# Performance work log

Measured on AMD Instinct MI355X. Metric: run time of the kernel, lower is better.

The kernel has to match this reference:

```python
import jax, jax.numpy as jnp
import numpy as np

N_HEAD, D_MODEL, D_K, D_V, MAX_NEIGHBOR = 8, 512, 64, 64, 5
BS, SEQ = 2, 1024


def setup_inputs() -> dict:
    key = jax.random.key(0)
    ks = jax.random.split(key, 12)
    inp = {
        'q': jax.random.normal(ks[0], (BS, SEQ, D_MODEL), jnp.float32),
        'k': jax.random.normal(ks[1], (BS, SEQ, D_MODEL), jnp.float32),
        'v': jax.random.normal(ks[2], (BS, SEQ, D_MODEL), jnp.float32),
        'mask': jnp.ones((BS, SEQ, SEQ), jnp.int32),
        'dist': jax.random.randint(ks[3], (BS, SEQ, SEQ), 0, 10, jnp.int32),
        # weights stored as (in, out) so y = x @ W
        'w_qs': jax.random.normal(ks[4], (D_MODEL, N_HEAD * D_K), jnp.float32) * 0.02,
        'w_ks': jax.random.normal(ks[5], (D_MODEL, N_HEAD * D_K), jnp.float32) * 0.02,
        'w_vs': jax.random.normal(ks[6], (D_MODEL, N_HEAD * D_V), jnp.float32) * 0.02,
        'w_fc': jax.random.normal(ks[7], (N_HEAD * D_V, D_MODEL), jnp.float32) * 0.02,
        'ln_gamma': jnp.ones((D_MODEL,), jnp.float32),
        'ln_beta': jnp.zeros((D_MODEL,), jnp.float32),
        'base_rpr': jax.random.normal(ks[8], (MAX_NEIGHBOR + 1, D_K), jnp.float32) * 0.02,
    }
    return inp


def reference(q, k, v, mask, dist, w_qs, w_ks, w_vs, w_fc, ln_gamma, ln_beta, base_rpr):
    bs, sq, dm = q.shape
    temp = jnp.asarray(D_K, q.dtype) ** 0.5
    residual = q
    # layer norm on q only (as in original)
    mu = jnp.mean(q, axis=-1, keepdims=True)
    var = jnp.var(q, axis=-1, keepdims=True)
    qn = (q - mu) / jnp.sqrt(var + 1e-6) * ln_gamma + ln_beta
    # projections -> [bs, heads, seq, d]
    qh = (qn @ w_qs).reshape(bs, sq, N_HEAD, D_K).transpose(0, 2, 1, 3)
    kh = (k @ w_ks).reshape(bs, sq, N_HEAD, D_K).transpose(0, 2, 1, 3)
    vh = (v @ w_vs).reshape(bs, sq, N_HEAD, D_V).transpose(0, 2, 1, 3)
    qs = qh / temp
    # standard QK^T scores
    attn1 = jnp.einsum('bhid,bhjd->bhij', qs, kh)
    # relative-position scores: instead of materializing rpr[b,i,j,d],
    # contract q with the small base table then gather by clipped distance.
    dc = jnp.minimum(dist, MAX_NEIGHBOR)  # dist>max_neighbor -> max_neighbor
    qb = jnp.einsum('bhid,md->bhim', qs, base_rpr)  # [bs,h,seq,M+1]
    idx = jnp.broadcast_to(dc[:, None, :, :], (bs, N_HEAD, sq, sq))
    attn2 = jnp.take_along_axis(qb, idx, axis=-1)  # [bs,h,seq,seq]
    attn = attn1 + attn2
    attn = jnp.where(mask[:, None, :, :] == 0, jnp.asarray(-1e9, attn.dtype), attn)
    attn = jax.nn.softmax(attn, axis=-1)  # dropout disabled (eval)
    out = jnp.einsum('bhij,bhjd->bhid', attn, vh)
    out = out.transpose(0, 2, 1, 3).reshape(bs, sq, N_HEAD * D_V)
    out = out @ w_fc + residual
    return out, attn
```

## Files before the change

### kernel.cpp

```cpp
#include <hip/hip_runtime.h>
#include <math.h>

#define SEQ 1024
#define DM 512

typedef __attribute__((ext_vector_type(8))) short bf16x8;
typedef __attribute__((ext_vector_type(4))) short bf16x4;
typedef __attribute__((ext_vector_type(4))) float f32x4;
typedef __attribute__((ext_vector_type(4))) int i32x4;
typedef __attribute__((ext_vector_type(2))) unsigned int u32x2;

static __device__ __forceinline__ short f2b(float f) {
    union { float f; unsigned u; } x; x.f = f;
    unsigned r = (x.u + 0x7FFFu + ((x.u >> 16) & 1u)) >> 16;
    return (short)r;
}
static __device__ __forceinline__ float b2f(short s) {
    union { unsigned u; float f; } x; x.u = ((unsigned)(unsigned short)s) << 16;
    return x.f;
}
static __device__ __forceinline__ int sidx(int row, int col) {
    int byte = (row << 7) + (col << 1);
    byte ^= (row & 7) << 4;
    return byte >> 1;
}
static __device__ __forceinline__ int svidx(int row, int m) {
    int byte = (row << 6) + (m << 1);
    byte ^= (row & 7) << 4;
    return byte >> 1;
}
static __device__ __forceinline__ int spidx(int row, int m) {
    int byte = (row << 6) | (m << 1);
    byte ^= ((row >> 2) & 3) << 4;
    return byte >> 1;
}

static __device__ __forceinline__ void stage_f32(short* dst, const float* src, int srcStride, int tid) {
    int r = tid >> 2, c = (tid & 3) * 16;
    const float* p = src + (size_t)r * srcStride + c;
    bf16x8 v0, v1;
    #pragma unroll
    for (int e = 0; e < 8; ++e) v0[e] = f2b(p[e]);
    #pragma unroll
    for (int e = 0; e < 8; ++e) v1[e] = f2b(p[8 + e]);
    *(bf16x8*)&dst[sidx(r, c)] = v0;
    *(bf16x8*)&dst[sidx(r, c + 8)] = v1;
}
static __device__ __forceinline__ void stage_bf16(short* dst, const short* src, int srcStride, int tid) {
    int r = tid >> 2, c = (tid & 3) * 16;
    const short* p = src + (size_t)r * srcStride + c;
    bf16x8 v0 = *(const bf16x8*)p;
    bf16x8 v1 = *(const bf16x8*)(p + 8);
    *(bf16x8*)&dst[sidx(r, c)] = v0;
    *(bf16x8*)&dst[sidx(r, c + 8)] = v1;
}

static __device__ __forceinline__ void mma64(const short* sA, const short* sB, f32x4* acc,
                                             int w, int lr, int lg) {
    #pragma unroll
    for (int ks = 0; ks < 2; ++ks) {
        bf16x8 af = *(const bf16x8*)&sA[sidx(w * 16 + lr, ks * 32 + lg * 8)];
        #pragma unroll
        for (int nt = 0; nt < 4; ++nt) {
            bf16x8 bf = *(const bf16x8*)&sB[sidx(nt * 16 + lr, ks * 32 + lg * 8)];
            acc[nt] = __builtin_amdgcn_mfma_f32_16x16x32_bf16(af, bf, acc[nt], 0, 0, 0);
        }
    }
}

__global__ __launch_bounds__(256) void prep_kernel(
    const float* __restrict__ w0, const float* __restrict__ w1,
    const float* __restrict__ w2, const float* __restrict__ w3, short* __restrict__ wt,
    const float* __restrict__ q, float* __restrict__ qn,
    const float* __restrict__ gamma, const float* __restrict__ beta,
    const int* __restrict__ dist, const int* __restrict__ mask, unsigned char* __restrict__ idxp) {
    int blk = blockIdx.x;
    int tid = threadIdx.x;
    if (blk < 256) {
        int wsel = blk >> 6;
        int t = blk & 63;
        int tr = t >> 3, tc = t & 7;
        const float* src = wsel == 0 ? w0 : wsel == 1 ? w1 : wsel == 2 ? w2 : w3;
        short* dst = wt + (size_t)wsel * 512 * 512;
        __shared__ float tile[64][65];
        int r = tid >> 2, c = (tid & 3) * 16;
        const float* p = src + (size_t)(tr * 64 + r) * 512 + tc * 64 + c;
        #pragma unroll
        for (int e = 0; e < 16; ++e) tile[r][c + e] = p[e];
        __syncthreads();
        bf16x8 v0, v1;
        #pragma unroll
        for (int e = 0; e < 16; ++e) {
            short bv = f2b(tile[c + e][r]);
            if (e < 8) v0[e] = bv; else v1[e - 8] = bv;
        }
        short* qd = dst + (size_t)(tc * 64 + r) * 512 + tr * 64 + c;
        *(bf16x8*)qd = v0;
        *(bf16x8*)(qd + 8) = v1;
    } else if (blk < 2304) {
        int row = blk - 256;
        const float* x = q + (size_t)row * DM;
        float* y = qn + (size_t)row * DM;
        float v1 = x[tid], v2 = x[tid + 256];
        float s = v1 + v2;
        float ss = v1 * v1 + v2 * v2;
        for (int o = 32; o > 0; o >>= 1) { s += __shfl_down(s, o); ss += __shfl_down(ss, o); }
        __shared__ float red[4], red2[4];
        __shared__ float s_mu, s_rstd;
        int wid = tid >> 6, lane = tid & 63;
        if (lane == 0) { red[wid] = s; red2[wid] = ss; }
        __syncthreads();
        if (tid == 0) {
            float ts = red[0] + red[1] + red[2] + red[3];
            float tss = red2[0] + red2[1] + red2[2] + red2[3];
            float mu = ts / DM;
            float var = tss / DM - mu * mu;
            s_mu = mu;
            s_rstd = rsqrtf(var + 1e-6f);
        }
        __syncthreads();
        float mu = s_mu, rstd = s_rstd;
        y[tid]       = (v1 - mu) * rstd * gamma[tid]       + beta[tid];
        y[tid + 256] = (v2 - mu) * rstd * gamma[tid + 256] + beta[tid + 256];
    } else {
        size_t base = ((size_t)(blk - 2304) * 256 + tid) * 4;
        i32x4 dv = *(const i32x4*)(dist + base);
        i32x4 mv = *(const i32x4*)(mask + base);
        unsigned char out[4];
        #pragma unroll
        for (int e = 0; e < 4; ++e) {
            int dc = dv[e]; dc = dc > 5 ? 5 : dc;
            out[e] = (unsigned char)(dc | (mv[e] == 0 ? 8 : 0));
        }
        *(uchar4*)(idxp + base) = *(uchar4*)out;
    }
}

__global__ __launch_bounds__(256) void qkv_kernel(
    const float* __restrict__ qn, const float* __restrict__ k, const float* __restrict__ v,
    const short* __restrict__ wT, short* __restrict__ qsb, short* __restrict__ khb,
    short* __restrict__ vT) {
    __shared__ short sA[64 * 64];
    __shared__ short sB[64 * 64];
    int tid = threadIdx.x;
    int sel = blockIdx.x >> 8;
    int t = blockIdx.x & 255;
    int bx = t & 7, by = t >> 3;
    int m0 = by << 6, n0 = bx << 6;
    int w = tid >> 6, l = tid & 63;
    int lr = l & 15, lg = l >> 4;
    const float* A = sel == 0 ? qn : sel == 1 ? k : v;
    const short* Bt = wT + (size_t)sel * 262144;
    float scale = sel == 0 ? 0.125f : 1.0f;
    f32x4 acc[4] = {};
    for (int kt = 0; kt < 512; kt += 64) {
        __syncthreads();
        stage_f32(sA, A + (size_t)m0 * 512 + kt, 512, tid);
        stage_bf16(sB, Bt + (size_t)n0 * 512 + kt, 512, tid);
        __syncthreads();
        mma64(sA, sB, acc, w, lr, lg);
    }
    if (sel == 2) {
        #pragma unroll
        for (int nt = 0; nt < 4; ++nt) {
            int gn = n0 + nt * 16 + lr;
            int gm0 = m0 + w * 16 + lg * 4;
            int bq = gm0 >> 10, j0 = gm0 & 1023;
            int h = gn >> 6, dl = gn & 63;
            bf16x4 pk;
            #pragma unroll
            for (int r = 0; r < 4; ++r) pk[r] = f2b(acc[nt][r]);
            *(bf16x4*)&vT[(((size_t)((bq << 3) + h) << 6) + dl) * 1024 + j0] = pk;
        }
    } else {
        short* C = sel == 0 ? qsb : khb;
        #pragma unroll
        for (int nt = 0; nt < 4; ++nt) {
            #pragma unroll
            for (int r = 0; r < 4; ++r) {
                int gm = m0 + w * 16 + lg * 4 + r;
                int gn = n0 + nt * 16 + lr;
                C[(size_t)gm * 512 + gn] = f2b(acc[nt][r] * scale);
            }
        }
    }
}

#define IDXSTR 1040
__global__ __launch_bounds__(256) void attn_fused_kernel(
    const short* __restrict__ qsb, const short* __restrict__ khb,
    const short* __restrict__ vT, const unsigned char* __restrict__ idxp,
    const float* __restrict__ rpr, float* __restrict__ attnp, short* __restrict__ oh) {
    int bid = blockIdx.x;
    int bh = bid >> 6, it = bid & 63;
    int b = bh >> 3, h = bh & 7;
    int i0 = it << 4;
    int tid = threadIdx.x;
    int w = tid >> 6, l = tid & 63;
    int lr = l & 15, lg = l >> 4;

    __shared__ short sQ[16 * 64];
    __shared__ short sPw[4 * 512];
    __shared__ float sQB[16 * 8];
    __shared__ float sL[4][16];
    __shared__ __align__(16) char sScr[4 * 6144];
    __shared__ __align__(16) unsigned char sIdx[16 * IDXSTR];

    short* sKw = (short*)(sScr + w * 6144);
    short* sVw = (short*)(sScr + w * 6144 + 2048);
    if (tid < 128) {
        int r = tid >> 3, c = (tid & 7) * 8;
        bf16x8 qv = *(const bf16x8*)(qsb + ((size_t)(b * SEQ + i0 + r)) * DM + h * 64 + c);
        *(bf16x8*)&sQ[sidx(r, c)] = qv;
    }
    {
        const unsigned char* ibase = idxp + ((size_t)(b * SEQ + i0)) * SEQ;
        #pragma unroll
        for (int p = 0; p < 4; ++p) {
            int row = p * 4 + (tid >> 6);
            int cb = (tid & 63) * 16;
            i32x4 v = *(const i32x4*)(ibase + (size_t)row * SEQ + cb);
            *(i32x4*)&sIdx[row * IDXSTR + cb] = v;
        }
    }
    __syncthreads();
    if (tid < 128) {
        int r = tid >> 3, m = tid & 7;
        if (m < 6) {
            float a = 0.f;
            #pragma unroll 8
            for (int d = 0; d < 64; ++d) a += b2f(sQ[sidx(r, d)]) * rpr[m * 64 + d];
            sQB[r * 8 + m] = a;
        }
    }
    __syncthreads();

    bf16x8 qf0 = *(const bf16x8*)&sQ[sidx(lr, lg * 8)];
    bf16x8 qf1 = *(const bf16x8*)&sQ[sidx(lr, 32 + lg * 8)];

    float l_acc[4] = {0.f, 0.f, 0.f, 0.f};
    unsigned p_lo[16], p_hi[16];
    f32x4 accO[4] = {};
    short* pw = sPw + w * 512;
    const short* kbase = khb + ((size_t)(b * SEQ)) * DM + h * 64;
    const short* vbase = vT + ((size_t)(bh * 64)) * 1024;

    #pragma unroll
    for (int jt = 0; jt < 16; ++jt) {
        {
            const short* kg = kbase + (size_t)(jt * 64 + w * 16) * DM;
            int sr = l >> 3, sc = (l & 7) * 8;
            bf16x8 t0 = *(const bf16x8*)(kg + (size_t)sr * DM + sc);
            bf16x8 t1 = *(const bf16x8*)(kg + (size_t)(8 + sr) * DM + sc);
            *(bf16x8*)&sKw[sidx(sr, sc)] = t0;
            *(bf16x8*)&sKw[sidx(8 + sr, sc)] = t1;
        }
        if (!(jt & 1)) {
            #pragma unroll
            for (int i = 0; i < 4; ++i) {
                int d = (i & 1) * 32 + (l >> 1);
                int jtX = jt + (i >> 1);
                int col = jtX * 64 + w * 16 + (l & 1) * 8;
                bf16x8 tv = *(const bf16x8*)(vbase + (size_t)d * 1024 + col);
                *(bf16x8*)&sVw[svidx(d, (i >> 1) * 16 + (l & 1) * 8)] = tv;
            }
        }
        bf16x8 kf0 = *(const bf16x8*)&sKw[sidx(lr, lg * 8)];
        bf16x8 kf1 = *(const bf16x8*)&sKw[sidx(lr, 32 + lg * 8)];
        f32x4 sf = {};
        sf = __builtin_amdgcn_mfma_f32_16x16x32_bf16(qf0, kf0, sf, 0, 0, 0);
        sf = __builtin_amdgcn_mfma_f32_16x16x32_bf16(qf1, kf1, sf, 0, 0, 0);
        int jcol = jt * 64 + w * 16 + lr;
        float pv[4];
        #pragma unroll
        for (int r = 0; r < 4; ++r) {
            unsigned bb = sIdx[(lg * 4 + r) * IDXSTR + jcol];
            float s = fminf(sf[r] + sQB[(lg * 4 + r) * 8 + (bb & 7)], 30.f);
            float p = (bb & 8) ? 0.f : __expf(s);
            pv[r] = p;
            l_acc[r] += p;
        }
        unsigned plo = (unsigned)(unsigned short)f2b(pv[0]) | ((unsigned)(unsigned short)f2b(pv[1]) << 16);
        unsigned phi = (unsigned)(unsigned short)f2b(pv[2]) | ((unsigned)(unsigned short)f2b(pv[3]) << 16);
        p_lo[jt] = plo; p_hi[jt] = phi;
        int m = (jt & 1) * 16 + lr;
        pw[spidx(lg * 4 + 0, m)] = (short)(plo & 0xffff);
        pw[spidx(lg * 4 + 1, m)] = (short)(plo >> 16);
        pw[spidx(lg * 4 + 2, m)] = (short)(phi & 0xffff);
        pw[spidx(lg * 4 + 3, m)] = (short)(phi >> 16);
        if (jt & 1) {
            bf16x8 af = *(const bf16x8*)&pw[spidx(lr, lg * 8)];
            #pragma unroll
            for (int nt = 0; nt < 4; ++nt) {
                bf16x8 bf = *(const bf16x8*)&sVw[svidx(nt * 16 + lr, lg * 8)];
                accO[nt] = __builtin_amdgcn_mfma_f32_16x16x32_bf16(af, bf, accO[nt], 0, 0, 0);
            }
        }
    }

    #pragma unroll
    for (int r = 0; r < 4; ++r) {
        float s = l_acc[r];
        s += __shfl_xor(s, 1); s += __shfl_xor(s, 2);
        s += __shfl_xor(s, 4); s += __shfl_xor(s, 8);
        l_acc[r] = s;
    }
    if (lr == 0) {
        #pragma unroll
        for (int r = 0; r < 4; ++r) sL[w][lg * 4 + r] = l_acc[r];
    }
    float* sOw = (float*)(sScr + w * 6144);
    #pragma unroll
    for (int nt = 0; nt < 4; ++nt)
        #pragma unroll
        for (int r = 0; r < 4; ++r)
            sOw[(lg * 4 + r) * 64 + nt * 16 + lr] = accO[nt][r];
    __syncthreads();

    {
        int row = tid >> 4, c4 = (tid & 15) * 4;
        f32x4 o = *(f32x4*)((float*)(sScr + 0 * 6144) + row * 64 + c4);
        o += *(f32x4*)((float*)(sScr + 1 * 6144) + row * 64 + c4);
        o += *(f32x4*)((float*)(sScr + 2 * 6144) + row * 64 + c4);
        o += *(f32x4*)((float*)(sScr + 3 * 6144) + row * 64 + c4);
        float rl = 1.f / (sL[0][row] + sL[1][row] + sL[2][row] + sL[3][row]);
        bf16x4 ob;
        #pragma unroll
        for (int e = 0; e < 4; ++e) ob[e] = f2b(o[e] * rl);
        *(bf16x4*)&oh[((size_t)(b * SEQ + i0 + row)) * DM + h * 64 + c4] = ob;
    }

    float rla[4];
    #pragma unroll
    for (int r = 0; r < 4; ++r) {
        int row = lg * 4 + r;
        rla[r] = 1.f / (sL[0][row] + sL[1][row] + sL[2][row] + sL[3][row]);
    }
    float* ap = attnp + ((size_t)(bh * SEQ + i0 + lg * 4)) * SEQ + w * 16 + lr;
    #pragma unroll
    for (int jt = 0; jt < 16; ++jt) {
        unsigned plo = p_lo[jt], phi = p_hi[jt];
        ap[(size_t)0 * SEQ + jt * 64] = b2f((short)(plo & 0xffff)) * rla[0];
        ap[(size_t)1 * SEQ + jt * 64] = b2f((short)(plo >> 16))    * rla[1];
        ap[(size_t)2 * SEQ + jt * 64] = b2f((short)(phi & 0xffff)) * rla[2];
        ap[(size_t)3 * SEQ + jt * 64] = b2f((short)(phi >> 16))    * rla[3];
    }
}

__global__ __launch_bounds__(256) void fc_kernel(
    const short* __restrict__ oh, const short* __restrict__ BtFc,
    const float* __restrict__ Rsd, float* __restrict__ Cp) {
    __shared__ short sA[64 * 64];
    __shared__ short sB[64 * 64];
    int tid = threadIdx.x;
    int bx = blockIdx.x & 7, by = blockIdx.x >> 3;
    int m0 = by << 6, n0 = bx << 6;
    int w = tid >> 6, l = tid & 63;
    int lr = l & 15, lg = l >> 4;
    f32x4 acc[4] = {};
    for (int kt = 0; kt < 512; kt += 64) {
        __syncthreads();
        stage_bf16(sA, oh + (size_t)m0 * 512 + kt, 512, tid);
        stage_bf16(sB, BtFc + (size_t)n0 * 512 + kt, 512, tid);
        __syncthreads();
        mma64(sA, sB, acc, w, lr, lg);
    }
    #pragma unroll
    for (int nt = 0; nt < 4; ++nt)
        #pragma unroll
        for (int r = 0; r < 4; ++r) {
            int gm = m0 + w * 16 + lg * 4 + r;
            int gn = n0 + nt * 16 + lr;
            Cp[(size_t)gm * 512 + gn] = acc[nt][r] + Rsd[(size_t)gm * 512 + gn];
        }
}

extern "C" void kernel_launch(void* const* d_in, const int* in_sizes, int n_in,
                              void* d_out, int out_size, void* d_ws, size_t ws_size,
                              hipStream_t stream) {
    const float* q     = (const float*)d_in[0];
    const float* k     = (const float*)d_in[1];
    const float* v     = (const float*)d_in[2];
    const int*   mask  = (const int*)d_in[3];
    const int*   dist  = (const int*)d_in[4];
    const float* w_qs  = (const float*)d_in[5];
    const float* w_ks  = (const float*)d_in[6];
    const float* w_vs  = (const float*)d_in[7];
    const float* w_fc  = (const float*)d_in[8];
    const float* gamma = (const float*)d_in[9];
    const float* beta  = (const float*)d_in[10];
    const float* rpr   = (const float*)d_in[11];

    char* wsb = (char*)d_ws;
    float* qn   = (float*)wsb;
    short* oh   = (short*)wsb;
    short* wT   = (short*)(wsb + 4u * 1024 * 1024);
    short* qsb  = (short*)(wsb + 6u * 1024 * 1024);
    short* khb  = (short*)(wsb + 8u * 1024 * 1024);
    short* vT   = (short*)(wsb + 10u * 1024 * 1024);
    unsigned char* idxp = (unsigned char*)(wsb + 12u * 1024 * 1024);

    float* outp  = (float*)d_out;
    float* attnp = outp + 1048576;

    prep_kernel<<<4352, 256, 0, stream>>>(w_qs, w_ks, w_vs, w_fc, wT, q, qn, gamma, beta, dist, mask, idxp);
    qkv_kernel<<<768, 256, 0, stream>>>(qn, k, v, wT, qsb, khb, vT);
    attn_fused_kernel<<<1024, 256, 0, stream>>>(qsb, khb, vT, idxp, rpr, attnp, oh);
    fc_kernel<<<256, 256, 0, stream>>>(oh, wT + 786432, q, outp);
}
```

Measured before the change: 74.31 us.

## Transpose score MFMA so P stays in registers and attn stores vectorize

Swaps the MFMA operands so each lane holds four consecutive key columns of one query row. This enables a single 32-bit index load, register-resident rpr bias selection via selects, a lane-local row sum, and 16-byte vectorized stores of the attention matrix. The LDS round-trip for P before the PV MFMA is replaced by cross-lane shuffles, and bf16 packing uses a hardware convert instruction. It trades LDS traffic and scattered 4-byte global stores for extra shuffles and selects, with a risk of mistakes in the operand layout mapping.

```diff
diff --git a/kernel.cpp b/kernel.cpp
--- a/kernel.cpp
+++ b/kernel.cpp
@@ -8,7 +8,6 @@
 typedef __attribute__((ext_vector_type(4))) short bf16x4;
 typedef __attribute__((ext_vector_type(4))) float f32x4;
 typedef __attribute__((ext_vector_type(4))) int i32x4;
-typedef __attribute__((ext_vector_type(2))) unsigned int u32x2;
 
 static __device__ __forceinline__ short f2b(float f) {
     union { float f; unsigned u; } x; x.f = f;
@@ -27,11 +26,6 @@
 static __device__ __forceinline__ int svidx(int row, int m) {
     int byte = (row << 6) + (m << 1);
     byte ^= (row & 7) << 4;
-    return byte >> 1;
-}
-static __device__ __forceinline__ int spidx(int row, int m) {
-    int byte = (row << 6) | (m << 1);
-    byte ^= ((row >> 2) & 3) << 4;
     return byte >> 1;
 }
 
@@ -200,7 +194,6 @@
     int lr = l & 15, lg = l >> 4;
 
     __shared__ short sQ[16 * 64];
-    __shared__ short sPw[4 * 512];
     __shared__ float sQB[16 * 8];
     __shared__ float sL[4][16];
     __shared__ __align__(16) char sScr[4 * 6144];
@@ -208,6 +201,7 @@
 
     short* sKw = (short*)(sScr + w * 6144);
     short* sVw = (short*)(sScr + w * 6144 + 2048);
+
     if (tid < 128) {
         int r = tid >> 3, c = (tid & 7) * 8;
         bf16x8 qv = *(const bf16x8*)(qsb + ((size_t)(b * SEQ + i0 + r)) * DM + h * 64 + c);
@@ -238,10 +232,12 @@
     bf16x8 qf0 = *(const bf16x8*)&sQ[sidx(lr, lg * 8)];
     bf16x8 qf1 = *(const bf16x8*)&sQ[sidx(lr, 32 + lg * 8)];
 
-    float l_acc[4] = {0.f, 0.f, 0.f, 0.f};
+    float qb0 = sQB[lr * 8 + 0], qb1 = sQB[lr * 8 + 1], qb2 = sQB[lr * 8 + 2];
+    float qb3 = sQB[lr * 8 + 3], qb4 = sQB[lr * 8 + 4], qb5 = sQB[lr * 8 + 5];
+
+    float l_lane = 0.f;
     unsigned p_lo[16], p_hi[16];
     f32x4 accO[4] = {};
-    short* pw = sPw + w * 512;
     const short* kbase = khb + ((size_t)(b * SEQ)) * DM + h * 64;
     const short* vbase = vT + ((size_t)(bh * 64)) * 1024;
 
@@ -268,28 +264,44 @@
         bf16x8 kf0 = *(const bf16x8*)&sKw[sidx(lr, lg * 8)];
         bf16x8 kf1 = *(const bf16x8*)&sKw[sidx(lr, 32 + lg * 8)];
         f32x4 sf = {};
-        sf = __builtin_amdgcn_mfma_f32_16x16x32_bf16(qf0, kf0, sf, 0, 0, 0);
-        sf = __builtin_amdgcn_mfma_f32_16x16x32_bf16(qf1, kf1, sf, 0, 0, 0);
-        int jcol = jt * 64 + w * 16 + lr;
+        sf = __builtin_amdgcn_mfma_f32_16x16x32_bf16(kf0, qf0, sf, 0, 0, 0);
+        sf = __builtin_amdgcn_mfma_f32_16x16x32_bf16(kf1, qf1, sf, 0, 0, 0);
+        int jcol0 = jt * 64 + w * 16 + lg * 4;
+        unsigned u = *(const unsigned*)&sIdx[lr * IDXSTR + jcol0];
         float pv[4];
         #pragma unroll
         for (int r = 0; r < 4; ++r) {
-            unsigned bb = sIdx[(lg * 4 + r) * IDXSTR + jcol];
-            float s = fminf(sf[r] + sQB[(lg * 4 + r) * 8 + (bb & 7)], 30.f);
+            unsigned bb = (u >> (8 * r)) & 0xffu;
+            unsigned dd = bb & 7u;
+            float t0 = (dd & 1) ? qb1 : qb0;
+            float t1 = (dd & 1) ? qb3 : qb2;
+            float t2 = (dd & 1) ? qb5 : qb4;
+            float u0 = (dd & 2) ? t1 : t0;
+            float bias = (dd & 4) ? t2 : u0;
+            float s = fminf(sf[r] + bias, 30.f);
             float p = (bb & 8) ? 0.f : __expf(s);
             pv[r] = p;
-            l_acc[r] += p;
-        }
-        unsigned plo = (unsigned)(unsigned short)f2b(pv[0]) | ((unsigned)(unsigned short)f2b(pv[1]) << 16);
-        unsigned phi = (unsigned)(unsigned short)f2b(pv[2]) | ((unsigned)(unsigned short)f2b(pv[3]) << 16);
+            l_lane += p;
+        }
+        unsigned plo, phi;
+        asm("v_cvt_pk_bf16_f32 %0, %1, %2" : "=v"(plo) : "v"(pv[0]), "v"(pv[1]));
+        asm("v_cvt_pk_bf16_f32 %0, %1, %2" : "=v"(phi) : "v"(pv[2]), "v"(pv[3]));
         p_lo[jt] = plo; p_hi[jt] = phi;
-        int m = (jt & 1) * 16 + lr;
-        pw[spidx(lg * 4 + 0, m)] = (short)(plo & 0xffff);
-        pw[spidx(lg * 4 + 1, m)] = (short)(plo >> 16);
-        pw[spidx(lg * 4 + 2, m)] = (short)(phi & 0xffff);
-        pw[spidx(lg * 4 + 3, m)] = (short)(phi >> 16);
         if (jt & 1) {
-            bf16x8 af = *(const bf16x8*)&pw[spidx(lr, lg * 8)];
+            unsigned plo0 = p_lo[jt - 1], phi0 = p_hi[jt - 1];
+            int srcA = lr + ((lg & 1) << 5);
+            int srcB = srcA + 16;
+            unsigned aw0 = __shfl(plo0, srcA), aw1 = __shfl(phi0, srcA);
+            unsigned aw2 = __shfl(plo,  srcA), aw3 = __shfl(phi,  srcA);
+            unsigned bw0 = __shfl(plo0, srcB), bw1 = __shfl(phi0, srcB);
+            unsigned bw2 = __shfl(plo,  srcB), bw3 = __shfl(phi,  srcB);
+            bool hi = lg >= 2;
+            union { unsigned q[4]; bf16x8 v; } afu;
+            afu.q[0] = hi ? aw2 : aw0;
+            afu.q[1] = hi ? aw3 : aw1;
+            afu.q[2] = hi ? bw2 : bw0;
+            afu.q[3] = hi ? bw3 : bw1;
+            bf16x8 af = afu.v;
             #pragma unroll
             for (int nt = 0; nt < 4; ++nt) {
                 bf16x8 bf = *(const bf16x8*)&sVw[svidx(nt * 16 + lr, lg * 8)];
@@ -298,17 +310,9 @@
         }
     }
 
-    #pragma unroll
-    for (int r = 0; r < 4; ++r) {
-        float s = l_acc[r];
-        s += __shfl_xor(s, 1); s += __shfl_xor(s, 2);
-        s += __shfl_xor(s, 4); s += __shfl_xor(s, 8);
-        l_acc[r] = s;
-    }
-    if (lr == 0) {
-        #pragma unroll
-        for (int r = 0; r < 4; ++r) sL[w][lg * 4 + r] = l_acc[r];
-    }
+    l_lane += __shfl_xor(l_lane, 16);
+    l_lane += __shfl_xor(l_lane, 32);
+    if (lg == 0) sL[w][lr] = l_lane;
     float* sOw = (float*)(sScr + w * 6144);
     #pragma unroll
     for (int nt = 0; nt < 4; ++nt)
@@ -330,20 +334,17 @@
         *(bf16x4*)&oh[((size_t)(b * SEQ + i0 + row)) * DM + h * 64 + c4] = ob;
     }
 
-    float rla[4];
-    #pragma unroll
-    for (int r = 0; r < 4; ++r) {
-        int row = lg * 4 + r;
-        rla[r] = 1.f / (sL[0][row] + sL[1][row] + sL[2][row] + sL[3][row]);
-    }
-    float* ap = attnp + ((size_t)(bh * SEQ + i0 + lg * 4)) * SEQ + w * 16 + lr;
+    float rl = 1.f / (sL[0][lr] + sL[1][lr] + sL[2][lr] + sL[3][lr]);
+    float* ap = attnp + ((size_t)(bh * SEQ + i0 + lr)) * SEQ + w * 16 + lg * 4;
     #pragma unroll
     for (int jt = 0; jt < 16; ++jt) {
         unsigned plo = p_lo[jt], phi = p_hi[jt];
-        ap[(size_t)0 * SEQ + jt * 64] = b2f((short)(plo & 0xffff)) * rla[0];
-        ap[(size_t)1 * SEQ + jt * 64] = b2f((short)(plo >> 16))    * rla[1];
-        ap[(size_t)2 * SEQ + jt * 64] = b2f((short)(phi & 0xffff)) * rla[2];
-        ap[(size_t)3 * SEQ + jt * 64] = b2f((short)(phi >> 16))    * rla[3];
+        f32x4 o;
+        o[0] = b2f((short)(plo & 0xffff)) * rl;
+        o[1] = b2f((short)(plo >> 16))    * rl;
+        o[2] = b2f((short)(phi & 0xffff)) * rl;
+        o[3] = b2f((short)(phi >> 16))    * rl;
+        *(f32x4*)&ap[jt * 64] = o;
     }
 }
 
```

After: 72.81 us. 2.0% less time.
